# Kernel tuning notes

Measured on AMD Instinct MI355X. Metric: run time of the kernel, lower is better.

Reference implementation:

```python
import jax, jax.numpy as jnp
import numpy as np

NBINS_PIX = 256   # uint8 pixel values
NBINS_MEAN = 512  # neighbor mean fits in [0, 408] for side=1


def setup_inputs() -> dict:
    key = jax.random.key(0)
    # uniform [0,1) so x.max() < 1.0 branch (x*255 quantization) is taken, as in the source
    x = jax.random.uniform(key, (64, 1024, 1024), dtype=jnp.float32)
    return {"x": x}


def reference(x):
    H, W = x.shape[-2:]
    x = jax.lax.stop_gradient(x)  # mirrors .clone().detach()
    xf = x.reshape(-1, H, W)
    B = xf.shape[0]
    # quantize: (x*255).to(uint8) if max<1 else x.to(uint8); uint8 cast truncates
    scale = jnp.where(jnp.max(xf) < 1.0, jnp.float32(255.0), jnp.float32(1.0))
    xq = (xf * scale).astype(jnp.uint8).astype(jnp.float32)
    xi = xq.astype(jnp.int32)

    # zero-padded 8-neighbor sum (3x3 window minus center), side=1
    xp = jnp.pad(xi, ((0, 0), (1, 1), (1, 1)))
    nb = jnp.zeros_like(xi)
    for dh in range(3):
        for dw in range(3):
            if dh == 1 and dw == 1:
                continue
            nb = nb + xp[:, dh:dh + H, dw:dw + W]

    # Faithful replication of the source's normalization: the original indexes
    # mean_nb[a, b] where dim0 is the BATCH dim and dim1 is the row dim, so the
    # divisor depends on (batch, row) and broadcasts over columns.
    # t=0: num=3 at 4 (batch,row) corners; then num->5 for edges and interior.
    D = jnp.ones((B, H), dtype=jnp.float32)
    D = D.at[0, 0].set(3.0).at[-1, 0].set(3.0).at[0, -1].set(3.0).at[-1, -1].set(3.0)
    D = D.at[1:-1, 0].set(5.0).at[1:-1, -1].set(5.0)
    D = D.at[0, 1:-1].set(5.0).at[-1, 1:-1].set(5.0)
    D = D.at[1:-1, 1:-1].set(5.0)
    mean_nb = nb.astype(jnp.float32) / D[:, :, None]
    mean_i = mean_nb.astype(jnp.int32)  # trunc toward zero, values >= 0

    # joint (pixel, mean) histogram per image -> entropy, matches unique+counts
    codes = xi * NBINS_MEAN + mean_i  # in [0, 256*512)

    def hist_entropy(c):
        counts = jnp.zeros(NBINS_PIX * NBINS_MEAN, jnp.float32).at[c.reshape(-1)].add(1.0)
        p = counts / (H * W)
        safe = jnp.where(p > 0, p, 1.0)
        return jnp.sum(jnp.where(p > 0, -p * jnp.log2(safe), 0.0))

    ent = jax.vmap(hist_entropy)(codes)  # [B]
    return jnp.mean(ent)
```

## Files before the change

### kernel.cpp

```cpp
#include <hip/hip_runtime.h>

#define IMG_H 1024
#define IMG_W 1024
#define NPIX  (IMG_H * IMG_W)
#define NBINS (256 * 512)
#define TILE  64
#define LW    (TILE + 2)

#define MEANS  428
#define HBINS  (256 * MEANS)
#define HWORDS (HBINS / 4)
#define QUADS  4
#define QROWS  (IMG_H / QUADS)

__global__ __launch_bounds__(1024) void fused_hist_kernel(const float* __restrict__ x,
                                                          unsigned int* __restrict__ partials,
                                                          int B) {
    __shared__ unsigned int h[HWORDS];

    const int blk  = blockIdx.x;
    const int b    = blk >> 2;
    const int quad = blk & 3;
    const int t    = threadIdx.x;

    for (int i = t; i < HWORDS; i += 1024) h[i] = 0u;
    __syncthreads();

    const float* img = x + (size_t)b * NPIX;
    const int rs = quad * QROWS;
    const bool bEdge = (b == 0) || (b == B - 1);

    const int cl = (t > 0) ? t - 1 : 0;
    const int cr = (t < IMG_W - 1) ? t + 1 : IMG_W - 1;

    auto loadrow = [&](int r, float& pL, float& pC, float& pR) {
        if ((unsigned)r < IMG_H) {
            const float* row = img + r * IMG_W;
            pL = row[cl]; pC = row[t]; pR = row[cr];
        } else { pL = 0.0f; pC = 0.0f; pR = 0.0f; }
    };
    auto qhsum = [&](float pL, float pC, float pR, int& hs, int& qc) {
        int qL = (int)(pL * 255.0f);
        int qC = (int)(pC * 255.0f);
        int qR = (int)(pR * 255.0f);
        if (t == 0)         qL = 0;
        if (t == IMG_W - 1) qR = 0;
        qc = qC; hs = qL + qC + qR;
    };

    int hA, hB, qB;
    { float a, m, c; loadrow(rs - 1, a, m, c); int qq; qhsum(a, m, c, hA, qq); }
    { float a, m, c; loadrow(rs,     a, m, c); qhsum(a, m, c, hB, qB); }
    float nL, nC, nR; loadrow(rs + 1, nL, nC, nR);

    for (int r = rs; r < rs + QROWS; ++r) {
        float cL = nL, cC = nC, cR = nR;
        loadrow(r + 2, nL, nC, nR);
        int hC, qC; qhsum(cL, cC, cR, hC, qC);

        int nb = hA + hB + hC - qB;
        unsigned mean;
        if (bEdge && (r == 0 || r == IMG_H - 1)) mean = (unsigned)nb / 3u;
        else                                     mean = (unsigned)nb / 5u;

        unsigned bin = (unsigned)qB * MEANS + mean;
        atomicAdd(&h[bin >> 2], 1u << ((bin & 3u) * 8u));

        hA = hB; hB = hC; qB = qC;
    }
    __syncthreads();

    unsigned int* dst = partials + (size_t)blk * HWORDS;
    for (int i = t; i < HWORDS; i += 1024) dst[i] = h[i];
}

__global__ __launch_bounds__(256) void merge_entropy_kernel(const unsigned int* __restrict__ partials,
                                                            double* __restrict__ acc,
                                                            int B) {
    double local = 0.0;
    const int n = B * HWORDS;
    for (int idx = blockIdx.x * 256 + threadIdx.x; idx < n; idx += gridDim.x * 256) {
        int img = idx / HWORDS;
        int w   = idx - img * HWORDS;
        const unsigned int* p = partials + (size_t)img * QUADS * HWORDS + w;
        unsigned w0 = p[0], w1 = p[HWORDS], w2 = p[2 * HWORDS], w3 = p[3 * HWORDS];
#pragma unroll
        for (int sh = 0; sh < 32; sh += 8) {
            unsigned c = ((w0 >> sh) & 255u) + ((w1 >> sh) & 255u)
                       + ((w2 >> sh) & 255u) + ((w3 >> sh) & 255u);
            if (c) local += (double)c * (20.0 - (double)log2f((float)c));
        }
    }
    for (int off = 32; off > 0; off >>= 1)
        local += __shfl_down(local, off, 64);

    __shared__ double sacc[4];
    const int lane = threadIdx.x & 63;
    const int wid  = threadIdx.x >> 6;
    if (lane == 0) sacc[wid] = local;
    __syncthreads();
    if (threadIdx.x == 0)
        atomicAdd(acc, sacc[0] + sacc[1] + sacc[2] + sacc[3]);
}

__global__ void finalize_kernel(const double* __restrict__ acc,
                                float* __restrict__ out, int B) {
    out[0] = (float)(acc[0] / ((double)NPIX * (double)B));
}

__global__ __launch_bounds__(256) void hist_kernel(const float* __restrict__ x,
                                                   unsigned int* __restrict__ hist,
                                                   int B) {
    __shared__ int s[LW * LW];
    const int tilesPerRow = IMG_W / TILE;
    const int tilesPerImg = (IMG_H / TILE) * tilesPerRow;
    const int b   = blockIdx.x / tilesPerImg;
    const int t   = blockIdx.x % tilesPerImg;
    const int ty0 = (t / tilesPerRow) * TILE;
    const int tx0 = (t % tilesPerRow) * TILE;
    const float* img = x + (size_t)b * NPIX;
    const int tid = threadIdx.x;

    for (int i = tid; i < LW * LW; i += 256) {
        int r = i / LW, c = i - r * LW;
        int gy = ty0 + r - 1, gx = tx0 + c - 1;
        int v = 0;
        if ((unsigned)gy < IMG_H && (unsigned)gx < IMG_W)
            v = (int)(img[gy * IMG_W + gx] * 255.0f);
        s[i] = v;
    }
    __syncthreads();

    unsigned int* hb = hist + (size_t)b * NBINS;
    const bool bEdge = (b == 0) || (b == B - 1);
    const int tx = tid & 63, sy = tid >> 6;
    const int c = tx + 1, r0 = sy * 16;

    int h0, h1, m1;
    { int a = s[r0 * LW + c - 1], m = s[r0 * LW + c], d = s[r0 * LW + c + 1]; h0 = a + m + d; }
    { int a = s[(r0 + 1) * LW + c - 1], m = s[(r0 + 1) * LW + c], d = s[(r0 + 1) * LW + c + 1]; h1 = a + m + d; m1 = m; }

    for (int ry = r0; ry < r0 + 16; ++ry) {
        int a = s[(ry + 2) * LW + c - 1], m = s[(ry + 2) * LW + c], d = s[(ry + 2) * LW + c + 1];
        int h2 = a + m + d;
        int nb = h0 + h1 + h2 - m1;
        int gy = ty0 + ry;
        unsigned mean = (unsigned)nb / 5u;
        if (bEdge && (gy == 0 || gy == IMG_H - 1)) mean = (unsigned)nb / 3u;
        atomicAdd(&hb[m1 * 512 + (int)mean], 1u);
        h0 = h1; h1 = h2; m1 = m;
    }
}

__global__ __launch_bounds__(256) void entropy_kernel(const unsigned int* __restrict__ hist,
                                                      double* __restrict__ acc, int n) {
    double local = 0.0;
    const int stride = gridDim.x * 256;
    for (int i = blockIdx.x * 256 + threadIdx.x; i < n; i += stride) {
        unsigned int cv = hist[i];
        if (cv) local += (double)cv * (20.0 - (double)log2f((float)cv));
    }
    for (int off = 32; off > 0; off >>= 1)
        local += __shfl_down(local, off, 64);
    __shared__ double sacc[4];
    const int lane = threadIdx.x & 63, wid = threadIdx.x >> 6;
    if (lane == 0) sacc[wid] = local;
    __syncthreads();
    if (threadIdx.x == 0)
        atomicAdd(acc, sacc[0] + sacc[1] + sacc[2] + sacc[3]);
}

extern "C" void kernel_launch(void* const* d_in, const int* in_sizes, int n_in,
                              void* d_out, int out_size, void* d_ws, size_t ws_size,
                              hipStream_t stream) {
    const float* x = (const float*)d_in[0];
    const int B = in_sizes[0] / NPIX;

    const size_t partBytes = (size_t)B * QUADS * HWORDS * sizeof(unsigned int);

    if (ws_size >= partBytes + 64) {
        unsigned int* partials = (unsigned int*)d_ws;
        double* acc = (double*)((char*)d_ws + partBytes);
        hipMemsetAsync(acc, 0, sizeof(double), stream);

        fused_hist_kernel<<<B * QUADS, 1024, 0, stream>>>(x, partials, B);
        merge_entropy_kernel<<<256, 256, 0, stream>>>(partials, acc, B);
        finalize_kernel<<<1, 1, 0, stream>>>(acc, (float*)d_out, B);
    } else {
        unsigned int* hist = (unsigned int*)d_ws;
        const size_t histBytes = (size_t)B * NBINS * sizeof(unsigned int);
        double* acc = (double*)((char*)d_ws + histBytes);
        hipMemsetAsync(d_ws, 0, histBytes + sizeof(double), stream);

        const int tilesPerImg = (IMG_H / TILE) * (IMG_W / TILE);
        hist_kernel<<<B * tilesPerImg, 256, 0, stream>>>(x, hist, B);
        entropy_kernel<<<1024, 256, 0, stream>>>(hist, acc, B * NBINS);
        finalize_kernel<<<1, 1, 0, stream>>>(acc, (float*)d_out, B);
    }
}
```

Baseline: 482.8 us.

## Vectorize histogram kernel to four columns per thread and flatten merge grid

Each thread in the fused histogram kernel now processes four adjacent columns via a float4 load plus two halo loads, with the block split into four row strips instead of each thread walking a full quarter-image column. The merge kernel uses a 2D grid with one packed word per thread, removing the grid-stride loop and integer division. This aims to cut global load instructions and address math, at the cost of extra halo rows per strip and more registers.

New measurement: 454.6 us. 5.8% less time.

```diff
diff --git a/kernel.cpp b/kernel.cpp
--- a/kernel.cpp
+++ b/kernel.cpp
@@ -21,75 +21,89 @@
     const int blk  = blockIdx.x;
     const int b    = blk >> 2;
     const int quad = blk & 3;
-    const int t    = threadIdx.x;
-
-    for (int i = t; i < HWORDS; i += 1024) h[i] = 0u;
+    const int tid  = threadIdx.x;
+
+    for (int i = tid; i < HWORDS; i += 1024) h[i] = 0u;
     __syncthreads();
 
     const float* img = x + (size_t)b * NPIX;
-    const int rs = quad * QROWS;
+    const int c0    = (tid & 255) * 4;
+    const int strip = tid >> 8;
+    const int rs    = quad * QROWS + strip * (QROWS / 4);
+    const int re    = rs + QROWS / 4;
     const bool bEdge = (b == 0) || (b == B - 1);
 
-    const int cl = (t > 0) ? t - 1 : 0;
-    const int cr = (t < IMG_W - 1) ? t + 1 : IMG_W - 1;
-
-    auto loadrow = [&](int r, float& pL, float& pC, float& pR) {
+    auto loadraw = [&](int r, float4& f, float& fl, float& fr) {
         if ((unsigned)r < IMG_H) {
             const float* row = img + r * IMG_W;
-            pL = row[cl]; pC = row[t]; pR = row[cr];
-        } else { pL = 0.0f; pC = 0.0f; pR = 0.0f; }
+            f  = *(const float4*)(row + c0);
+            fl = (c0 > 0) ? row[c0 - 1] : 0.0f;
+            fr = (c0 + 4 < IMG_W) ? row[c0 + 4] : 0.0f;
+        } else { f = make_float4(0.f, 0.f, 0.f, 0.f); fl = 0.f; fr = 0.f; }
     };
-    auto qhsum = [&](float pL, float pC, float pR, int& hs, int& qc) {
-        int qL = (int)(pL * 255.0f);
-        int qC = (int)(pC * 255.0f);
-        int qR = (int)(pR * 255.0f);
-        if (t == 0)         qL = 0;
-        if (t == IMG_W - 1) qR = 0;
-        qc = qC; hs = qL + qC + qR;
+    auto quant6 = [&](const float4& f, float fl, float fr, int q[6]) {
+        q[0] = (int)(fl  * 255.0f);
+        q[1] = (int)(f.x * 255.0f);
+        q[2] = (int)(f.y * 255.0f);
+        q[3] = (int)(f.z * 255.0f);
+        q[4] = (int)(f.w * 255.0f);
+        q[5] = (int)(fr  * 255.0f);
     };
 
-    int hA, hB, qB;
-    { float a, m, c; loadrow(rs - 1, a, m, c); int qq; qhsum(a, m, c, hA, qq); }
-    { float a, m, c; loadrow(rs,     a, m, c); qhsum(a, m, c, hB, qB); }
-    float nL, nC, nR; loadrow(rs + 1, nL, nC, nR);
-
-    for (int r = rs; r < rs + QROWS; ++r) {
-        float cL = nL, cC = nC, cR = nR;
-        loadrow(r + 2, nL, nC, nR);
-        int hC, qC; qhsum(cL, cC, cR, hC, qC);
-
-        int nb = hA + hB + hC - qB;
-        unsigned mean;
-        if (bEdge && (r == 0 || r == IMG_H - 1)) mean = (unsigned)nb / 3u;
-        else                                     mean = (unsigned)nb / 5u;
-
-        unsigned bin = (unsigned)qB * MEANS + mean;
-        atomicAdd(&h[bin >> 2], 1u << ((bin & 3u) * 8u));
-
-        hA = hB; hB = hC; qB = qC;
+    int hA[4], hB[4], qB[4];
+    {
+        float4 f; float fl, fr; loadraw(rs - 1, f, fl, fr);
+        int q[6]; quant6(f, fl, fr, q);
+#pragma unroll
+        for (int i = 0; i < 4; ++i) hA[i] = q[i] + q[i + 1] + q[i + 2];
+    }
+    {
+        float4 f; float fl, fr; loadraw(rs, f, fl, fr);
+        int q[6]; quant6(f, fl, fr, q);
+#pragma unroll
+        for (int i = 0; i < 4; ++i) { hB[i] = q[i] + q[i + 1] + q[i + 2]; qB[i] = q[i + 1]; }
+    }
+    float4 pf; float pfl, pfr; loadraw(rs + 1, pf, pfl, pfr);
+
+    for (int r = rs; r < re; ++r) {
+        float4 cf = pf; float cfl = pfl, cfr = pfr;
+        loadraw(r + 2, pf, pfl, pfr);
+
+        int q[6]; quant6(cf, cfl, cfr, q);
+        int hC[4];
+#pragma unroll
+        for (int i = 0; i < 4; ++i) hC[i] = q[i] + q[i + 1] + q[i + 2];
+
+        const bool corner = bEdge && (r == 0 || r == IMG_H - 1);
+#pragma unroll
+        for (int i = 0; i < 4; ++i) {
+            int nb = hA[i] + hB[i] + hC[i] - qB[i];
+            unsigned mean = corner ? (unsigned)nb / 3u : (unsigned)nb / 5u;
+            unsigned bin  = (unsigned)qB[i] * MEANS + mean;
+            atomicAdd(&h[bin >> 2], 1u << ((bin & 3u) * 8u));
+            hA[i] = hB[i]; hB[i] = hC[i]; qB[i] = q[i + 1];
+        }
     }
     __syncthreads();
 
     unsigned int* dst = partials + (size_t)blk * HWORDS;
-    for (int i = t; i < HWORDS; i += 1024) dst[i] = h[i];
+    for (int i = tid; i < HWORDS; i += 1024) dst[i] = h[i];
 }
 
 __global__ __launch_bounds__(256) void merge_entropy_kernel(const unsigned int* __restrict__ partials,
                                                             double* __restrict__ acc,
                                                             int B) {
+    const int w   = blockIdx.x * 256 + threadIdx.x;
+    const int img = blockIdx.y;
+    const unsigned int* p = partials + (size_t)img * QUADS * HWORDS + w;
+    unsigned w0 = p[0], w1 = p[HWORDS], w2 = p[2 * HWORDS], w3 = p[3 * HWORDS];
+
     double local = 0.0;
-    const int n = B * HWORDS;
-    for (int idx = blockIdx.x * 256 + threadIdx.x; idx < n; idx += gridDim.x * 256) {
-        int img = idx / HWORDS;
-        int w   = idx - img * HWORDS;
-        const unsigned int* p = partials + (size_t)img * QUADS * HWORDS + w;
-        unsigned w0 = p[0], w1 = p[HWORDS], w2 = p[2 * HWORDS], w3 = p[3 * HWORDS];
-#pragma unroll
-        for (int sh = 0; sh < 32; sh += 8) {
-            unsigned c = ((w0 >> sh) & 255u) + ((w1 >> sh) & 255u)
-                       + ((w2 >> sh) & 255u) + ((w3 >> sh) & 255u);
-            if (c) local += (double)c * (20.0 - (double)log2f((float)c));
-        }
+#pragma unroll
+    for (int sh = 0; sh < 32; sh += 8) {
+        unsigned c = ((w0 >> sh) & 255u) + ((w1 >> sh) & 255u)
+                   + ((w2 >> sh) & 255u) + ((w3 >> sh) & 255u);
+        if (c) local += (double)c * (20.0 - (double)log2f((float)c));
     }
     for (int off = 32; off > 0; off >>= 1)
         local += __shfl_down(local, off, 64);
@@ -184,7 +198,7 @@
         hipMemsetAsync(acc, 0, sizeof(double), stream);
 
         fused_hist_kernel<<<B * QUADS, 1024, 0, stream>>>(x, partials, B);
-        merge_entropy_kernel<<<256, 256, 0, stream>>>(partials, acc, B);
+        merge_entropy_kernel<<<dim3(HWORDS / 256, B), 256, 0, stream>>>(partials, acc, B);
         finalize_kernel<<<1, 1, 0, stream>>>(acc, (float*)d_out, B);
     } else {
         unsigned int* hist = (unsigned int*)d_ws;
```
